# Performance work log

Hardware: AMD Instinct MI355X
Metric: run time of the kernel (lower is better)

The kernel has to match this reference:

```python
import jax, jax.numpy as jnp
import numpy as np
from jax import lax

N = 1_000_000   # nodes
E = 16_000_000  # edges
K1, K2, K3 = 100_000, 10_000, 2_500  # ceil(ratio*n) per pooling stage
EPS = 1e-5


def cgconv(x, src, dst, edge_attr, edge_valid, Wf, bf, Ws, bs, gamma, beta, num_nodes):
    # z_ij = [x_i, x_j, e_ij]  (PyG: i = target = dst, j = source = src)
    z = jnp.concatenate([x[dst], x[src], edge_attr], axis=-1)          # [E,3]
    m = jax.nn.sigmoid(z @ Wf + bf) * jax.nn.softplus(z @ Ws + bs)     # [E,1]
    m = m * edge_valid[:, None].astype(m.dtype)
    aggr = jax.ops.segment_sum(m, dst, num_segments=num_nodes)         # [n,1]
    # BatchNorm1d (training-mode batch stats, biased var), then residual
    mean = aggr.mean(axis=0)
    var = aggr.var(axis=0)
    bn = gamma * (aggr - mean) / jnp.sqrt(var + EPS) + beta
    return bn + x


def topk_pool(x, src, dst, edge_attr, edge_valid, w, k, num_nodes):
    # Original torch code broadcasts x[N,1]*w[C] -> sum(-1) == x*sum(w); tanh nonlinearity.
    score = jnp.tanh(x[:, 0] * jnp.sum(w) / jnp.linalg.norm(w))        # [n]
    top_scores, perm = lax.top_k(score, k)
    x_new = x[perm] * top_scores[:, None]
    mask = jnp.zeros((num_nodes,), bool).at[perm].set(True)
    new_idx = jnp.zeros((num_nodes,), jnp.int32).at[perm].set(jnp.arange(k, dtype=jnp.int32))
    ev = edge_valid & mask[src] & mask[dst]
    return x_new, new_idx[src], new_idx[dst], edge_attr, ev


def setup_inputs() -> dict:
    key = jax.random.key(0)
    ks = jax.random.split(key, 24)
    d = {}
    d["x"] = jax.random.normal(ks[0], (N, 1), jnp.float32)
    d["edge_attr"] = jax.random.uniform(ks[1], (E, 1), jnp.float32)
    d["src"] = jax.random.randint(ks[2], (E,), 0, N, jnp.int32)
    d["dst"] = jax.random.randint(ks[3], (E,), 0, N, jnp.int32)
    d["batch"] = jnp.zeros((N,), jnp.int32)
    p = lambda k, shp: jax.random.normal(k, shp, jnp.float32) * 0.1
    d["Wf1"], d["bf1"] = p(ks[4], (3, 1)), p(ks[5], (1,))
    d["Ws1"], d["bs1"] = p(ks[6], (3, 1)), p(ks[7], (1,))
    d["g1"], d["be1"] = jnp.ones((1,), jnp.float32), jnp.zeros((1,), jnp.float32)
    d["Wf2"], d["bf2"] = p(ks[8], (3, 1)), p(ks[9], (1,))
    d["Ws2"], d["bs2"] = p(ks[10], (3, 1)), p(ks[11], (1,))
    d["g2"], d["be2"] = jnp.ones((1,), jnp.float32), jnp.zeros((1,), jnp.float32)
    d["pw1"] = p(ks[12], (800,))
    d["pw2"] = p(ks[13], (80,))
    d["pw3"] = p(ks[14], (8,))
    d["Wl1"], d["bl1"] = p(ks[15], (1, 8)), p(ks[16], (8,))
    d["Wl2"], d["bl2"] = p(ks[17], (8, 2)), p(ks[18], (2,))
    return d


def reference(x, edge_attr, Wf1, bf1, Ws1, bs1, g1, be1, Wf2, bf2, Ws2, bs2, g2, be2,
              pw1, pw2, pw3, Wl1, bl1, Wl2, bl2, src, dst, batch):
    ev = jnp.ones((E,), bool)
    x = cgconv(x, src, dst, edge_attr, ev, Wf1, bf1, Ws1, bs1, g1, be1, N)
    x, s, dd, ea, ev = topk_pool(x, src, dst, edge_attr, ev, pw1, K1, N)
    x = cgconv(x, s, dd, ea, ev, Wf2, bf2, Ws2, bs2, g2, be2, K1)
    x, s, dd, ea, ev = topk_pool(x, s, dd, ea, ev, pw2, K2, K1)
    x, s, dd, ea, ev = topk_pool(x, s, dd, ea, ev, pw3, K3, K2)
    h = jax.nn.relu(x @ Wl1 + bl1)
    # dropout is identity in eval/reference mode
    return jax.nn.log_softmax(h @ Wl2 + bl2, axis=1)
```

## Files before the change

### kernel.cpp

```cpp
#include <hip/hip_runtime.h>
#include <math.h>

#define CHUNK 4096
#define NB2   256
#define BSH   12
#define CAP   24
#define CAPW  49
#define FG    16
#define RND   1024
#define EPB   16384

typedef int      i32x4 __attribute__((ext_vector_type(4)));
typedef float    f32x4 __attribute__((ext_vector_type(4)));
typedef unsigned u32x2 __attribute__((ext_vector_type(2)));

__device__ __forceinline__ i32x4 ntld4i(const int* p)   { return __builtin_nontemporal_load((const i32x4*)p); }
__device__ __forceinline__ f32x4 ntld4f(const float* p) { return __builtin_nontemporal_load((const f32x4*)p); }

__device__ __forceinline__ float sigmoidf_(float x) {
    if (x >= 0.0f) { float e = expf(-x); return 1.0f / (1.0f + e); }
    float e = expf(x); return e / (1.0f + e);
}
__device__ __forceinline__ float softplusf_(float x) {
    return fmaxf(x, 0.0f) + log1pf(expf(-fabsf(x)));
}
__device__ __forceinline__ unsigned key_desc(float f) {
    unsigned u = __float_as_uint(f);
    unsigned ka = (u & 0x80000000u) ? ~u : (u | 0x80000000u);
    return ~ka;
}
__device__ __forceinline__ float edge_m(float xd, float xs, float a,
                                        float wf0, float wf1, float wf2, float b0,
                                        float ws0, float ws1, float ws2, float b1) {
    float f = xd * wf0 + xs * wf1 + a * wf2 + b0;
    float g = xd * ws0 + xs * ws1 + a * ws2 + b1;
    return sigmoidf_(f) * softplusf_(g);
}

__global__ void k_consts(const float* __restrict__ pw1, const float* __restrict__ pw2,
                         const float* __restrict__ pw3, float* __restrict__ consts,
                         float* __restrict__ stats, int n1, int n2, int n3) {
    if (blockIdx.x == 0 && threadIdx.x < 16) stats[threadIdx.x] = 0.f;
    const float* w; int n;
    if (blockIdx.x == 0)      { w = pw1; n = n1; }
    else if (blockIdx.x == 1) { w = pw2; n = n2; }
    else                      { w = pw3; n = n3; }
    __shared__ float s1[256], s2[256];
    float a = 0.f, b = 0.f;
    for (int i = threadIdx.x; i < n; i += 256) { float v = w[i]; a += v; b += v * v; }
    s1[threadIdx.x] = a; s2[threadIdx.x] = b; __syncthreads();
    for (int o = 128; o > 0; o >>= 1) {
        if (threadIdx.x < o) { s1[threadIdx.x] += s1[threadIdx.x + o]; s2[threadIdx.x] += s2[threadIdx.x + o]; }
        __syncthreads();
    }
    if (threadIdx.x == 0) consts[blockIdx.x] = s1[0] / sqrtf(s2[0]);
}

__global__ void __launch_bounds__(256) k_ehist2(const int* __restrict__ dst,
                                                unsigned* __restrict__ hist,
                                                int e0, int e1) {
    __shared__ unsigned h[NB2];
    int t = threadIdx.x;
    h[t] = 0;
    __syncthreads();
    int cs = e0 + blockIdx.x * EPB;
    int ce = cs + EPB; if (ce > e1) ce = e1;
    for (int eb = cs; eb < ce; eb += RND) {
        int i = eb + t * 4;
        if (eb + RND <= ce) {
            i32x4 d4 = ntld4i(dst + i);
            atomicAdd(&h[((unsigned)d4.x) >> BSH], 1u);
            atomicAdd(&h[((unsigned)d4.y) >> BSH], 1u);
            atomicAdd(&h[((unsigned)d4.z) >> BSH], 1u);
            atomicAdd(&h[((unsigned)d4.w) >> BSH], 1u);
        } else {
            #pragma unroll
            for (int j = 0; j < 4; ++j)
                if (i + j < ce) atomicAdd(&h[((unsigned)dst[i + j]) >> BSH], 1u);
        }
    }
    __syncthreads();
    hist[(size_t)blockIdx.x * NB2 + t] = h[t];
}

__global__ void k_scanA(const unsigned* __restrict__ hist, unsigned* __restrict__ offs,
                        unsigned* __restrict__ tot, int G) {
    int d = blockIdx.x, ND = gridDim.x, t = threadIdx.x;
    __shared__ unsigned s[256];
    unsigned carry = 0;
    for (int tile = 0; tile * 256 < G; ++tile) {
        int g = tile * 256 + t;
        unsigned v = (g < G) ? hist[(size_t)g * ND + d] : 0u;
        s[t] = v; __syncthreads();
        for (int o = 1; o < 256; o <<= 1) {
            unsigned u = (t >= o) ? s[t - o] : 0u;
            __syncthreads();
            s[t] += u; __syncthreads();
        }
        if (g < G) offs[(size_t)g * ND + d] = s[t] - v + carry;
        unsigned tl = s[255]; __syncthreads();
        carry += tl;
    }
    if (t == 0) tot[d] = carry;
}

__global__ void __launch_bounds__(256) k_part(
        const float* __restrict__ x, const float* __restrict__ ea,
        const int* __restrict__ src, const int* __restrict__ dst,
        const float* __restrict__ Wf, const float* __restrict__ bf,
        const float* __restrict__ Ws, const float* __restrict__ bs,
        const unsigned* __restrict__ offs, const unsigned* __restrict__ tot,
        uint2* __restrict__ rec, int e0, int e1) {
    __shared__ unsigned stage[NB2 * CAPW];
    __shared__ unsigned gcur[NB2], fil[NB2];
    int t = threadIdx.x;
    {
        unsigned v = (tot[t] + FG - 1) & ~(unsigned)(FG - 1);
        stage[t] = v; __syncthreads();
        for (int o = 1; o < 256; o <<= 1) {
            unsigned u = (t >= o) ? stage[t - o] : 0u;
            __syncthreads();
            stage[t] += u; __syncthreads();
        }
        gcur[t] = (stage[t] - v) + offs[(size_t)blockIdx.x * NB2 + t];
        fil[t] = 0;
    }
    __syncthreads();
    int cs = e0 + blockIdx.x * EPB;
    int ce = cs + EPB; if (ce > e1) ce = e1;
    float wf0 = Wf[0], wf1 = Wf[1], wf2 = Wf[2], b0 = bf[0];
    float ws0 = Ws[0], ws1 = Ws[1], ws2 = Ws[2], b1 = bs[0];
    int sg = t >> 4, ln = t & 15;
    for (int rb = cs; rb < ce; rb += RND) {
        int s4[4], d4[4]; float a4[4]; bool vl[4];
        int eb = rb + t * 4;
        if (rb + RND <= ce) {
            i32x4 sv = ntld4i(src + eb);
            i32x4 dv = ntld4i(dst + eb);
            f32x4 av = ntld4f(ea + eb);
            s4[0]=sv.x; s4[1]=sv.y; s4[2]=sv.z; s4[3]=sv.w;
            d4[0]=dv.x; d4[1]=dv.y; d4[2]=dv.z; d4[3]=dv.w;
            a4[0]=av.x; a4[1]=av.y; a4[2]=av.z; a4[3]=av.w;
            vl[0]=vl[1]=vl[2]=vl[3]=true;
        } else {
            #pragma unroll
            for (int j = 0; j < 4; ++j) {
                int e = eb + j;
                vl[j] = e < ce;
                s4[j] = vl[j] ? src[e] : 0;
                d4[j] = vl[j] ? dst[e] : 0;
                a4[j] = vl[j] ? ea[e]  : 0.f;
            }
        }
        #pragma unroll
        for (int j = 0; j < 4; ++j) {
            if (!vl[j]) continue;
            int d = d4[j];
            float m = edge_m(x[d], x[s4[j]], a4[j], wf0, wf1, wf2, b0, ws0, ws1, ws2, b1);
            unsigned bin = ((unsigned)d) >> BSH;
            unsigned dl  = (unsigned)(d & ((1 << BSH) - 1));
            unsigned slot = atomicAdd(&fil[bin], 1u);
            if (slot < CAP) {
                stage[bin * CAPW + 2 * slot]     = __float_as_uint(m);
                stage[bin * CAPW + 2 * slot + 1] = dl;
            } else {
                rec[gcur[bin] + slot] = make_uint2(__float_as_uint(m), dl);
            }
        }
        __syncthreads();
        for (int i = 0; i < NB2 / 16; ++i) {
            int b = sg + (i << 4);
            unsigned c = fil[b];
            if (c < FG) continue;
            unsigned g = gcur[b];
            unsigned* st = &stage[b * CAPW];
            if (c > CAP) {
                rec[g + ln] = make_uint2(st[2 * ln], st[2 * ln + 1]);
                if (ln < CAP - 16)
                    rec[g + 16 + ln] = make_uint2(st[2 * (16 + ln)], st[2 * (16 + ln) + 1]);
                if (ln == 0) { gcur[b] = g + c; fil[b] = 0; }
            } else {
                rec[g + ln] = make_uint2(st[2 * ln], st[2 * ln + 1]);
                unsigned rem = c - FG;
                unsigned lo0 = 0, lo1 = 0;
                if (ln < rem) { lo0 = st[2 * (FG + ln)]; lo1 = st[2 * (FG + ln) + 1]; }
                if (ln < rem) { st[2 * ln] = lo0; st[2 * ln + 1] = lo1; }
                if (ln == 0) { gcur[b] = g + FG; fil[b] = rem; }
            }
        }
        __syncthreads();
    }
    for (int i = 0; i < NB2 / 16; ++i) {
        int b = sg + (i << 4);
        unsigned c = fil[b], g = gcur[b];
        unsigned* st = &stage[b * CAPW];
        if (ln < c) rec[g + ln] = make_uint2(st[2 * ln], st[2 * ln + 1]);
    }
}

__global__ void __launch_bounds__(256) k_aggr2(
        const uint2* __restrict__ rec, const unsigned* __restrict__ tot,
        float* __restrict__ aggr, float* __restrict__ stats,
        int N, int accumulate, int doStats) {
    __shared__ float acc[1 << BSH];
    __shared__ unsigned sc[256];
    __shared__ unsigned sBase, sCnt;
    int t = threadIdx.x, b = blockIdx.x;
    {
        unsigned v = (tot[t] + FG - 1) & ~(unsigned)(FG - 1);
        sc[t] = v; __syncthreads();
        for (int o = 1; o < 256; o <<= 1) {
            unsigned u = (t >= o) ? sc[t - o] : 0u;
            __syncthreads();
            sc[t] += u; __syncthreads();
        }
        if (t == b) { sBase = sc[t] - v; sCnt = tot[t]; }
    }
    for (int i = t; i < (1 << BSH); i += 256) acc[i] = 0.f;
    __syncthreads();
    unsigned lo = sBase, hi = lo + sCnt;
    for (unsigned i = lo + t; i < hi; i += 256) {
        u32x2 r = __builtin_nontemporal_load((const u32x2*)&rec[i]);
        atomicAdd(&acc[r.y], __uint_as_float(r.x));
    }
    __syncthreads();
    int nb = b << BSH;
    float s = 0.f, q = 0.f;
    for (int i = t; i < (1 << BSH); i += 256) {
        int node = nb + i;
        if (node < N) {
            float v = acc[i];
            if (accumulate) v += aggr[node];
            aggr[node] = v;
            if (doStats) { s += v; q += v * v; }
        }
    }
    if (doStats) {
        __shared__ float s1[256], s2[256];
        s1[t] = s; s2[t] = q; __syncthreads();
        for (int o = 128; o > 0; o >>= 1) {
            if (t < o) { s1[t] += s1[t + o]; s2[t] += s2[t + o]; }
            __syncthreads();
        }
        if (t == 0) { atomicAdd(&stats[0], s1[0]); atomicAdd(&stats[1], s2[0]); }
    }
}

__global__ void k_conv1(const float* __restrict__ x, const float* __restrict__ ea,
                        const int* __restrict__ src, const int* __restrict__ dst,
                        const float* __restrict__ Wf, const float* __restrict__ bf,
                        const float* __restrict__ Ws, const float* __restrict__ bs,
                        float* __restrict__ aggr, int E) {
    int e = blockIdx.x * blockDim.x + threadIdx.x;
    if (e >= E) return;
    int s = src[e], d = dst[e];
    atomicAdd(&aggr[d], edge_m(x[d], x[s], ea[e], Wf[0], Wf[1], Wf[2], bf[0],
                               Ws[0], Ws[1], Ws[2], bs[0]));
}

__global__ void __launch_bounds__(256) k_conv2(
        const float* __restrict__ x2, const float* __restrict__ ea,
        const int* __restrict__ src, const int* __restrict__ dst,
        const int* __restrict__ nidx,
        const float* __restrict__ Wf, const float* __restrict__ bf,
        const float* __restrict__ Ws, const float* __restrict__ bs,
        float* __restrict__ aggr, int E) {
    int base = (blockIdx.x * 256 + threadIdx.x) * 4;
    if (base >= E) return;
    float wf0 = Wf[0], wf1 = Wf[1], wf2 = Wf[2], b0 = bf[0];
    float ws0 = Ws[0], ws1 = Ws[1], ws2 = Ws[2], b1 = bs[0];
    int d4[4], s4[4]; int cnt;
    if (base + 4 <= E) {
        i32x4 dv = ntld4i(dst + base);
        i32x4 sv = ntld4i(src + base);
        d4[0]=dv.x; d4[1]=dv.y; d4[2]=dv.z; d4[3]=dv.w;
        s4[0]=sv.x; s4[1]=sv.y; s4[2]=sv.z; s4[3]=sv.w;
        cnt = 4;
    } else {
        cnt = E - base;
        for (int j = 0; j < cnt; ++j) { d4[j] = dst[base + j]; s4[j] = src[base + j]; }
    }
    #pragma unroll
    for (int j = 0; j < 4; ++j) {
        if (j >= cnt) break;
        int nd = nidx[d4[j]];
        if (nd < 0) continue;
        int ns = nidx[s4[j]];
        if (ns < 0) continue;
        float a = __builtin_nontemporal_load(ea + base + j);
        atomicAdd(&aggr[nd], edge_m(x2[nd], x2[ns], a, wf0, wf1, wf2, b0, ws0, ws1, ws2, b1));
    }
}

__global__ void k_stats(const float* __restrict__ a, int n, float* __restrict__ stats) {
    float s = 0.f, q = 0.f;
    int stride = gridDim.x * blockDim.x;
    for (int i = blockIdx.x * blockDim.x + threadIdx.x; i < n; i += stride) {
        float v = a[i]; s += v; q += v * v;
    }
    __shared__ float s1[256], s2[256];
    s1[threadIdx.x] = s; s2[threadIdx.x] = q; __syncthreads();
    for (int o = 128; o > 0; o >>= 1) {
        if (threadIdx.x < o) { s1[threadIdx.x] += s1[threadIdx.x + o]; s2[threadIdx.x] += s2[threadIdx.x + o]; }
        __syncthreads();
    }
    if (threadIdx.x == 0) { atomicAdd(&stats[0], s1[0]); atomicAdd(&stats[1], s2[0]); }
}

__global__ void k_bn(const float* __restrict__ aggr, const float* __restrict__ xin,
                     const float* __restrict__ stats, const float* __restrict__ g,
                     const float* __restrict__ be, float* __restrict__ xout,
                     int n, float invn, const float* __restrict__ consts, int ci,
                     unsigned* __restrict__ keys, unsigned* __restrict__ vals,
                     int* __restrict__ nidxInit, float* __restrict__ zeroArr, int nZero) {
    int i = blockIdx.x * blockDim.x + threadIdx.x;
    if (i >= n) return;
    if (nidxInit) nidxInit[i] = -1;
    if (zeroArr && i < nZero) zeroArr[i] = 0.f;
    float mean = stats[0] * invn;
    float var  = stats[1] * invn - mean * mean;
    float inv  = 1.0f / sqrtf(var + 1e-5f);
    float v = g[0] * (aggr[i] - mean) * inv + be[0] + xin[i];
    xout[i] = v;
    float s = tanhf(v * consts[ci]);
    keys[i] = key_desc(s);
    vals[i] = (unsigned)i;
}

__global__ void k_hist(const unsigned* __restrict__ keys, unsigned* __restrict__ hist,
                       int n, int shift) {
    __shared__ unsigned h[256];
    int t = threadIdx.x;
    h[t] = 0;
    __syncthreads();
    int base = blockIdx.x * CHUNK;
    if (base + CHUNK <= n) {
        #pragma unroll
        for (int it = 0; it < CHUNK / 1024; ++it) {
            int i = base + it * 1024 + t * 4;
            const unsigned* p = keys + i;
            unsigned k0 = p[0], k1 = p[1], k2 = p[2], k3 = p[3];
            atomicAdd(&h[(k0 >> shift) & 255u], 1u);
            atomicAdd(&h[(k1 >> shift) & 255u], 1u);
            atomicAdd(&h[(k2 >> shift) & 255u], 1u);
            atomicAdd(&h[(k3 >> shift) & 255u], 1u);
        }
    } else {
        for (int i = base + t; i < n; i += 256)
            atomicAdd(&h[(keys[i] >> shift) & 255u], 1u);
    }
    __syncthreads();
    hist[blockIdx.x * 256 + t] = h[t];
}

__global__ void __launch_bounds__(256) k_scatter(const unsigned* __restrict__ keys,
                                                 const unsigned* __restrict__ vals,
                                                 unsigned* __restrict__ okeys,
                                                 unsigned* __restrict__ ovals,
                                                 const unsigned* __restrict__ offs,
                                                 const unsigned* __restrict__ tot,
                                                 int n, int shift) {
    __shared__ unsigned run[256];
    __shared__ unsigned offl[256];
    __shared__ unsigned wcnt[4][256];
    __shared__ unsigned wpre[4][256];
    __shared__ unsigned sc[256];
    int t = threadIdx.x;
    int wave = t >> 6, lane = t & 63;
    {
        unsigned v = tot[t];
        sc[t] = v; __syncthreads();
        for (int o = 1; o < 256; o <<= 1) {
            unsigned u = (t >= o) ? sc[t - o] : 0u;
            __syncthreads();
            sc[t] += u; __syncthreads();
        }
        offl[t] = offs[(size_t)blockIdx.x * 256 + t] + (sc[t] - v);
        run[t] = 0;
    }
    __syncthreads();
    int cbase = blockIdx.x * CHUNK;
    const int GROUPS = CHUNK / 256;
    for (int gix = 0; gix < GROUPS; ++gix) {
        int i = cbase + gix * 256 + t;
        bool active = i < n;
        unsigned k = active ? keys[i] : 0u;
        unsigned v = active ? vals[i] : 0u;
        unsigned d = (k >> shift) & 255u;
        unsigned long long amask = __ballot(active);
        unsigned long long bb[8];
        #pragma unroll
        for (int bit = 0; bit < 8; ++bit) bb[bit] = __ballot(active && ((d >> bit) & 1u));
        unsigned long long m = amask;
        #pragma unroll
        for (int bit = 0; bit < 8; ++bit) m &= ((d >> bit) & 1u) ? bb[bit] : ~bb[bit];
        unsigned rk = (unsigned)__popcll(m & ((1ull << lane) - 1ull));
        #pragma unroll
        for (int j = 0; j < 4; ++j) {
            unsigned dd = (unsigned)lane + j * 64u;
            unsigned long long mm = amask;
            #pragma unroll
            for (int bit = 0; bit < 8; ++bit) mm &= ((dd >> bit) & 1u) ? bb[bit] : ~bb[bit];
            wcnt[wave][dd] = (unsigned)__popcll(mm);
        }
        __syncthreads();
        {
            unsigned r = run[t];
            unsigned c0 = wcnt[0][t], c1 = wcnt[1][t], c2 = wcnt[2][t], c3 = wcnt[3][t];
            wpre[0][t] = r;
            wpre[1][t] = r + c0;
            wpre[2][t] = r + c0 + c1;
            wpre[3][t] = r + c0 + c1 + c2;
            run[t] = r + c0 + c1 + c2 + c3;
        }
        __syncthreads();
        if (active) {
            unsigned pos = offl[d] + wpre[wave][d] + rk;
            okeys[pos] = k;
            ovals[pos] = v;
        }
    }
}

__global__ void k_pool(const unsigned* __restrict__ perm, const float* __restrict__ xin,
                       const float* __restrict__ consts, int ci,
                       float* __restrict__ xout, int* __restrict__ newidx, int k,
                       unsigned* __restrict__ okeys, unsigned* __restrict__ ovals, int nci) {
    int r = blockIdx.x * blockDim.x + threadIdx.x;
    if (r >= k) return;
    unsigned p = perm[r];
    float xv = xin[p];
    float s = tanhf(xv * consts[ci]);
    float o = xv * s;
    xout[r] = o;
    if (newidx) newidx[p] = r;
    if (okeys) {
        float s2 = tanhf(o * consts[nci]);
        okeys[r] = key_desc(s2);
        ovals[r] = (unsigned)r;
    }
}

__global__ void __launch_bounds__(1024) k_smallsort(
        unsigned* __restrict__ kIn, unsigned* __restrict__ vIn,
        unsigned* __restrict__ kTmp, unsigned* __restrict__ vTmp,
        int n, int k3, const float* __restrict__ xin,
        const float* __restrict__ consts, int ci,
        const float* __restrict__ Wl1, const float* __restrict__ bl1,
        const float* __restrict__ Wl2, const float* __restrict__ bl2,
        float* __restrict__ out) {
    __shared__ unsigned hist[256], sc[256], run[256], offl[256];
    __shared__ unsigned wcnt[16][256];
    __shared__ unsigned wpre[16][256];
    int t = threadIdx.x;
    int wave = t >> 6, lane = t & 63;
    unsigned *ki = kIn, *vi = vIn, *ko = kTmp, *vo = vTmp;
    for (int p = 0; p < 4; ++p) {
        int shift = p * 8;
        if (t < 256) hist[t] = 0;
        __syncthreads();
        for (int i = t; i < n; i += 1024)
            atomicAdd(&hist[(ki[i] >> shift) & 255u], 1u);
        __syncthreads();
        if (t < 256) sc[t] = hist[t];
        __syncthreads();
        for (int o = 1; o < 256; o <<= 1) {
            unsigned u = 0;
            if (t < 256 && t >= o) u = sc[t - o];
            __syncthreads();
            if (t < 256) sc[t] += u;
            __syncthreads();
        }
        if (t < 256) { offl[t] = sc[t] - hist[t]; run[t] = 0; }
        __syncthreads();
        int G = (n + 1023) / 1024;
        for (int gix = 0; gix < G; ++gix) {
            int i = gix * 1024 + t;
            bool active = i < n;
            unsigned k = active ? ki[i] : 0u;
            unsigned v = active ? vi[i] : 0u;
            unsigned d = (k >> shift) & 255u;
            unsigned long long amask = __ballot(active);
            unsigned long long bb[8];
            #pragma unroll
            for (int bit = 0; bit < 8; ++bit) bb[bit] = __ballot(active && ((d >> bit) & 1u));
            unsigned long long m = amask;
            #pragma unroll
            for (int bit = 0; bit < 8; ++bit) m &= ((d >> bit) & 1u) ? bb[bit] : ~bb[bit];
            unsigned rk = (unsigned)__popcll(m & ((1ull << lane) - 1ull));
            #pragma unroll
            for (int j = 0; j < 4; ++j) {
                unsigned dd = (unsigned)lane + j * 64u;
                unsigned long long mm = amask;
                #pragma unroll
                for (int bit = 0; bit < 8; ++bit) mm &= ((dd >> bit) & 1u) ? bb[bit] : ~bb[bit];
                wcnt[wave][dd] = (unsigned)__popcll(mm);
            }
            __syncthreads();
            if (t < 256) {
                unsigned acc = run[t];
                #pragma unroll
                for (int w2 = 0; w2 < 16; ++w2) { wpre[w2][t] = acc; acc += wcnt[w2][t]; }
                run[t] = acc;
            }
            __syncthreads();
            if (active) {
                unsigned pos = offl[d] + wpre[wave][d] + rk;
                ko[pos] = k;
                vo[pos] = v;
            }
            __syncthreads();
        }
        unsigned* tp;
        tp = ki; ki = ko; ko = tp;
        tp = vi; vi = vo; vo = tp;
        __syncthreads();
    }
    float c = consts[ci];
    float b20 = bl2[0], b21 = bl2[1];
    for (int r = t; r < k3; r += 1024) {
        unsigned pidx = vIn[r];
        float xv = xin[pidx];
        float s = tanhf(xv * c);
        float o = xv * s;
        float l0 = b20, l1 = b21;
        #pragma unroll
        for (int j = 0; j < 8; ++j) {
            float h = fmaxf(o * Wl1[j] + bl1[j], 0.0f);
            l0 += h * Wl2[2 * j];
            l1 += h * Wl2[2 * j + 1];
        }
        float mx = fmaxf(l0, l1);
        float lse = mx + logf(expf(l0 - mx) + expf(l1 - mx));
        out[2 * r]     = l0 - lse;
        out[2 * r + 1] = l1 - lse;
    }
}

static void sort_pairs(hipStream_t stream, unsigned* kA, unsigned* vA,
                       unsigned* kB, unsigned* vB, unsigned* hist, unsigned* offs,
                       unsigned* tot, int n) {
    int G = (n + CHUNK - 1) / CHUNK;
    unsigned *ki = kA, *vi = vA, *ko = kB, *vo = vB;
    for (int p = 0; p < 4; ++p) {
        int shift = p * 8;
        k_hist<<<G, 256, 0, stream>>>(ki, hist, n, shift);
        k_scanA<<<256, 256, 0, stream>>>(hist, offs, tot, G);
        k_scatter<<<G, 256, 0, stream>>>(ki, vi, ko, vo, offs, tot, n, shift);
        unsigned* t;
        t = ki; ki = ko; ko = t;
        t = vi; vi = vo; vo = t;
    }
}

extern "C" void kernel_launch(void* const* d_in, const int* in_sizes, int n_in,
                              void* d_out, int out_size, void* d_ws, size_t ws_size,
                              hipStream_t stream) {
    const float* x   = (const float*)d_in[0];
    const float* ea  = (const float*)d_in[1];
    const int*   src = (const int*)d_in[2];
    const int*   dst = (const int*)d_in[3];
    const float *Wf1 = (const float*)d_in[5],  *bf1 = (const float*)d_in[6];
    const float *Ws1 = (const float*)d_in[7],  *bs1 = (const float*)d_in[8];
    const float *g1  = (const float*)d_in[9],  *be1 = (const float*)d_in[10];
    const float *Wf2 = (const float*)d_in[11], *bf2 = (const float*)d_in[12];
    const float *Ws2 = (const float*)d_in[13], *bs2 = (const float*)d_in[14];
    const float *g2  = (const float*)d_in[15], *be2 = (const float*)d_in[16];
    const float *pw1 = (const float*)d_in[17], *pw2 = (const float*)d_in[18], *pw3 = (const float*)d_in[19];
    const float *Wl1 = (const float*)d_in[20], *bl1 = (const float*)d_in[21];
    const float *Wl2 = (const float*)d_in[22], *bl2 = (const float*)d_in[23];

    const int N  = in_sizes[0];
    const int E  = in_sizes[1];
    const int K1 = 100000, K2 = 10000, K3 = 2500;

    size_t off = 0;
    auto alloc = [&](size_t bytes) { size_t o = off; off = (off + bytes + 255) & ~(size_t)255; return o; };
    char* ws = (char*)d_ws;
    size_t o_x1    = alloc((size_t)N * 4);
    size_t o_nidx  = alloc((size_t)N * 4);
    size_t o_stats = alloc(256);
    size_t o_const = alloc(256);
    size_t o_tot   = alloc(4096);
    size_t o_x2    = alloc((size_t)K1 * 4);
    size_t o_x3    = alloc((size_t)K1 * 4);
    size_t o_ag2   = alloc((size_t)K1 * 4);
    size_t o_x4    = alloc((size_t)K2 * 4);
    size_t o_ag1   = alloc((size_t)N * 4);
    size_t o_arena = off;

    int G1 = (N + CHUNK - 1) / CHUNK;
    size_t s_kA = 0;
    size_t s_vA = s_kA + (((size_t)N * 4 + 255) & ~(size_t)255);
    size_t s_kB = s_vA + (((size_t)N * 4 + 255) & ~(size_t)255);
    size_t s_vB = s_kB + (((size_t)N * 4 + 255) & ~(size_t)255);
    size_t s_h  = s_vB + (((size_t)N * 4 + 255) & ~(size_t)255);
    size_t s_o  = s_h  + (((size_t)G1 * 256 * 4 + 255) & ~(size_t)255);
    size_t sortSz = s_o + (size_t)G1 * 256 * 4;

    int H = 0, Eh = 0;
    size_t p_rec = 0, p_eh = 0, p_eo = 0;
    for (int h = 1; h <= 8; h <<= 1) {
        int eh_ = (E + h - 1) / h;
        eh_ = (eh_ + RND - 1) & ~(RND - 1);
        int gc_ = (eh_ + EPB - 1) / EPB;
        size_t recB = (((size_t)(eh_ + NB2 * FG) * 8) + 255) & ~(size_t)255;
        size_t ehB  = (((size_t)gc_ * NB2 * 4) + 255) & ~(size_t)255;
        size_t eoB  = (((size_t)gc_ * NB2 * 4) + 255) & ~(size_t)255;
        size_t partSz = recB + ehB + eoB;
        size_t arenaSz = partSz > sortSz ? partSz : sortSz;
        if (o_arena + arenaSz <= ws_size && N <= (NB2 << BSH)) {
            H = h; Eh = eh_;
            p_rec = 0; p_eh = p_rec + recB; p_eo = p_eh + ehB;
            break;
        }
    }

    float*    x1     = (float*)(ws + o_x1);
    int*      nidx   = (int*)(ws + o_nidx);
    float*    stats  = (float*)(ws + o_stats);
    float*    consts = (float*)(ws + o_const);
    unsigned* tot    = (unsigned*)(ws + o_tot);
    float*    x2     = (float*)(ws + o_x2);
    float*    x3     = (float*)(ws + o_x3);
    float*    aggr2  = (float*)(ws + o_ag2);
    float*    x4     = (float*)(ws + o_x4);
    float*    aggr1  = (float*)(ws + o_ag1);
    unsigned* kA     = (unsigned*)(ws + o_arena + s_kA);
    unsigned* vA     = (unsigned*)(ws + o_arena + s_vA);
    unsigned* kB     = (unsigned*)(ws + o_arena + s_kB);
    unsigned* vB     = (unsigned*)(ws + o_arena + s_vB);
    unsigned* hist   = (unsigned*)(ws + o_arena + s_h);
    unsigned* offs   = (unsigned*)(ws + o_arena + s_o);

    k_consts<<<3, 256, 0, stream>>>(pw1, pw2, pw3, consts, stats,
                                    in_sizes[17], in_sizes[18], in_sizes[19]);

    if (H > 0) {
        uint2*    rec = (uint2*)(ws + o_arena + p_rec);
        unsigned* eh  = (unsigned*)(ws + o_arena + p_eh);
        unsigned* eo  = (unsigned*)(ws + o_arena + p_eo);
        int NBN = (N + (1 << BSH) - 1) >> BSH;
        for (int h = 0; h < H; ++h) {
            int e0 = h * Eh;
            int e1 = e0 + Eh; if (e1 > E) e1 = E;
            if (e0 >= e1) break;
            int GCh = (e1 - e0 + EPB - 1) / EPB;
            k_ehist2<<<GCh, 256, 0, stream>>>(dst, eh, e0, e1);
            k_scanA<<<NB2, 256, 0, stream>>>(eh, eo, tot, GCh);
            k_part<<<GCh, 256, 0, stream>>>(x, ea, src, dst, Wf1, bf1, Ws1, bs1,
                                            eo, tot, rec, e0, e1);
            k_aggr2<<<NBN, 256, 0, stream>>>(rec, tot, aggr1, stats, N,
                                             h > 0, h == H - 1 ? 1 : 0);
        }
    } else {
        hipMemsetAsync(aggr1, 0, (size_t)N * 4, stream);
        k_conv1<<<(E + 255) / 256, 256, 0, stream>>>(x, ea, src, dst, Wf1, bf1, Ws1, bs1, aggr1, E);
        k_stats<<<1024, 256, 0, stream>>>(aggr1, N, stats);
    }
    k_bn<<<(N + 255) / 256, 256, 0, stream>>>(aggr1, x, stats, g1, be1, x1, N, 1.0f / (float)N,
                                              consts, 0, kA, vA, nidx, aggr2, K1);

    sort_pairs(stream, kA, vA, kB, vB, hist, offs, tot, N);
    k_pool<<<(K1 + 255) / 256, 256, 0, stream>>>(vA, x1, consts, 0, x2, nidx, K1,
                                                 (unsigned*)nullptr, (unsigned*)nullptr, 0);

    k_conv2<<<(E / 4 + 255) / 256, 256, 0, stream>>>(x2, ea, src, dst, nidx,
                                                     Wf2, bf2, Ws2, bs2, aggr2, E);
    k_stats<<<256, 256, 0, stream>>>(aggr2, K1, stats + 2);
    k_bn<<<(K1 + 255) / 256, 256, 0, stream>>>(aggr2, x2, stats + 2, g2, be2, x3, K1, 1.0f / (float)K1,
                                               consts, 1, kA, vA,
                                               (int*)nullptr, (float*)nullptr, 0);

    sort_pairs(stream, kA, vA, kB, vB, hist, offs, tot, K1);
    k_pool<<<(K2 + 255) / 256, 256, 0, stream>>>(vA, x3, consts, 1, x4, (int*)nullptr, K2,
                                                 kB, vB, 2);

    k_smallsort<<<1, 1024, 0, stream>>>(kB, vB, kA, vA, K2, K3, x4, consts, 2,
                                        Wl1, bl1, Wl2, bl2, (float*)d_out);
}
```

Before: 882.7 us.

## Prefilter top-K candidates by radix histogram before sorting, and worklist partition flushes

Before the stage-1 top-K selection, a coarse 11-bit histogram of the sort keys locates the bin that contains the K-th key. Only keys at or below that bin are compacted and then radix-sorted, with the element count read from device memory, so roughly K1-sized data is sorted instead of all N nodes. Separately, the edge partition kernel keeps a per-round worklist of full bins instead of scanning all 256 bins, and pads each per-block bin segment to FG with zero records. This adds several small kernels and pads the record buffer, but it is meant to sharply cut the cost of the full-N sort.

```diff
diff --git a/kernel.cpp b/kernel.cpp
--- a/kernel.cpp
+++ b/kernel.cpp
@@ -13,6 +13,7 @@
 typedef int      i32x4 __attribute__((ext_vector_type(4)));
 typedef float    f32x4 __attribute__((ext_vector_type(4)));
 typedef unsigned u32x2 __attribute__((ext_vector_type(2)));
+typedef unsigned u32x4 __attribute__((ext_vector_type(4)));
 
 __device__ __forceinline__ i32x4 ntld4i(const int* p)   { return __builtin_nontemporal_load((const i32x4*)p); }
 __device__ __forceinline__ f32x4 ntld4f(const float* p) { return __builtin_nontemporal_load((const f32x4*)p); }
@@ -39,8 +40,12 @@
 
 __global__ void k_consts(const float* __restrict__ pw1, const float* __restrict__ pw2,
                          const float* __restrict__ pw3, float* __restrict__ consts,
-                         float* __restrict__ stats, int n1, int n2, int n3) {
-    if (blockIdx.x == 0 && threadIdx.x < 16) stats[threadIdx.x] = 0.f;
+                         float* __restrict__ stats, unsigned* __restrict__ ghist,
+                         int n1, int n2, int n3) {
+    if (blockIdx.x == 0) {
+        if (threadIdx.x < 16) stats[threadIdx.x] = 0.f;
+        for (int i = threadIdx.x; i < 2048; i += 256) ghist[i] = 0u;
+    }
     const float* w; int n;
     if (blockIdx.x == 0)      { w = pw1; n = n1; }
     else if (blockIdx.x == 1) { w = pw2; n = n2; }
@@ -84,13 +89,13 @@
 }
 
 __global__ void k_scanA(const unsigned* __restrict__ hist, unsigned* __restrict__ offs,
-                        unsigned* __restrict__ tot, int G) {
+                        unsigned* __restrict__ tot, int G, unsigned rmask) {
     int d = blockIdx.x, ND = gridDim.x, t = threadIdx.x;
     __shared__ unsigned s[256];
     unsigned carry = 0;
     for (int tile = 0; tile * 256 < G; ++tile) {
         int g = tile * 256 + t;
-        unsigned v = (g < G) ? hist[(size_t)g * ND + d] : 0u;
+        unsigned v = (g < G) ? ((hist[(size_t)g * ND + d] + rmask) & ~rmask) : 0u;
         s[t] = v; __syncthreads();
         for (int o = 1; o < 256; o <<= 1) {
             unsigned u = (t >= o) ? s[t - o] : 0u;
@@ -110,20 +115,27 @@
         const float* __restrict__ Wf, const float* __restrict__ bf,
         const float* __restrict__ Ws, const float* __restrict__ bs,
         const unsigned* __restrict__ offs, const unsigned* __restrict__ tot,
+        const unsigned* __restrict__ eh,
         uint2* __restrict__ rec, int e0, int e1) {
     __shared__ unsigned stage[NB2 * CAPW];
-    __shared__ unsigned gcur[NB2], fil[NB2];
+    __shared__ unsigned gcur[NB2], fil[NB2], gend[NB2];
+    __shared__ unsigned short wl[2][NB2];
+    __shared__ unsigned wlc[2];
     int t = threadIdx.x;
     {
-        unsigned v = (tot[t] + FG - 1) & ~(unsigned)(FG - 1);
+        unsigned v = tot[t];
         stage[t] = v; __syncthreads();
         for (int o = 1; o < 256; o <<= 1) {
             unsigned u = (t >= o) ? stage[t - o] : 0u;
             __syncthreads();
             stage[t] += u; __syncthreads();
         }
-        gcur[t] = (stage[t] - v) + offs[(size_t)blockIdx.x * NB2 + t];
+        unsigned g0 = (stage[t] - v) + offs[(size_t)blockIdx.x * NB2 + t];
+        unsigned cnt = eh[(size_t)blockIdx.x * NB2 + t];
+        gcur[t] = g0;
+        gend[t] = g0 + ((cnt + FG - 1) & ~(unsigned)(FG - 1));
         fil[t] = 0;
+        if (t < 2) wlc[t] = 0;
     }
     __syncthreads();
     int cs = e0 + blockIdx.x * EPB;
@@ -131,7 +143,9 @@
     float wf0 = Wf[0], wf1 = Wf[1], wf2 = Wf[2], b0 = bf[0];
     float ws0 = Ws[0], ws1 = Ws[1], ws2 = Ws[2], b1 = bs[0];
     int sg = t >> 4, ln = t & 15;
-    for (int rb = cs; rb < ce; rb += RND) {
+    int rnd = 0;
+    for (int rb = cs; rb < ce; rb += RND, ++rnd) {
+        int cur = rnd & 1;
         int s4[4], d4[4]; float a4[4]; bool vl[4];
         int eb = rb + t * 4;
         if (rb + RND <= ce) {
@@ -160,6 +174,10 @@
             unsigned bin = ((unsigned)d) >> BSH;
             unsigned dl  = (unsigned)(d & ((1 << BSH) - 1));
             unsigned slot = atomicAdd(&fil[bin], 1u);
+            if (slot == FG - 1) {
+                unsigned w = atomicAdd(&wlc[cur], 1u);
+                wl[cur][w] = (unsigned short)bin;
+            }
             if (slot < CAP) {
                 stage[bin * CAPW + 2 * slot]     = __float_as_uint(m);
                 stage[bin * CAPW + 2 * slot + 1] = dl;
@@ -168,11 +186,10 @@
             }
         }
         __syncthreads();
-        for (int i = 0; i < NB2 / 16; ++i) {
-            int b = sg + (i << 4);
-            unsigned c = fil[b];
-            if (c < FG) continue;
-            unsigned g = gcur[b];
+        unsigned nw = wlc[cur];
+        for (unsigned i = sg; i < nw; i += 16) {
+            int b = wl[cur][i];
+            unsigned c = fil[b], g = gcur[b];
             unsigned* st = &stage[b * CAPW];
             if (c > CAP) {
                 rec[g + ln] = make_uint2(st[2 * ln], st[2 * ln + 1]);
@@ -182,19 +199,23 @@
             } else {
                 rec[g + ln] = make_uint2(st[2 * ln], st[2 * ln + 1]);
                 unsigned rem = c - FG;
-                unsigned lo0 = 0, lo1 = 0;
-                if (ln < rem) { lo0 = st[2 * (FG + ln)]; lo1 = st[2 * (FG + ln) + 1]; }
-                if (ln < rem) { st[2 * ln] = lo0; st[2 * ln + 1] = lo1; }
+                unsigned a0 = 0, a1 = 0;
+                if (ln < rem) { a0 = st[2 * (FG + ln)]; a1 = st[2 * (FG + ln) + 1]; }
+                if (ln < rem) { st[2 * ln] = a0; st[2 * ln + 1] = a1; }
                 if (ln == 0) { gcur[b] = g + FG; fil[b] = rem; }
             }
         }
+        if (t == 0) wlc[cur ^ 1] = 0;
         __syncthreads();
     }
     for (int i = 0; i < NB2 / 16; ++i) {
         int b = sg + (i << 4);
-        unsigned c = fil[b], g = gcur[b];
+        unsigned g = gcur[b], c = fil[b], ge = gend[b];
         unsigned* st = &stage[b * CAPW];
-        if (ln < c) rec[g + ln] = make_uint2(st[2 * ln], st[2 * ln + 1]);
+        for (unsigned p = g + ln; p < ge; p += 16) {
+            unsigned k2 = p - g;
+            rec[p] = (k2 < c) ? make_uint2(st[2 * k2], st[2 * k2 + 1]) : make_uint2(0u, 0u);
+        }
     }
 }
 
@@ -207,7 +228,7 @@
     __shared__ unsigned sBase, sCnt;
     int t = threadIdx.x, b = blockIdx.x;
     {
-        unsigned v = (tot[t] + FG - 1) & ~(unsigned)(FG - 1);
+        unsigned v = tot[t];
         sc[t] = v; __syncthreads();
         for (int o = 1; o < 256; o <<= 1) {
             unsigned u = (t >= o) ? sc[t - o] : 0u;
@@ -327,8 +348,106 @@
     vals[i] = (unsigned)i;
 }
 
+__global__ void __launch_bounds__(256) k_ghist(const unsigned* __restrict__ keys,
+                                               unsigned* __restrict__ ghist, int n) {
+    __shared__ unsigned h[2048];
+    int t = threadIdx.x;
+    for (int i = t; i < 2048; i += 256) h[i] = 0;
+    __syncthreads();
+    int stride = gridDim.x * 1024;
+    for (int base = blockIdx.x * 1024 + t * 4; base + 3 < n; base += stride) {
+        u32x4 k4 = __builtin_nontemporal_load((const u32x4*)(keys + base));
+        atomicAdd(&h[k4.x >> 21], 1u);
+        atomicAdd(&h[k4.y >> 21], 1u);
+        atomicAdd(&h[k4.z >> 21], 1u);
+        atomicAdd(&h[k4.w >> 21], 1u);
+    }
+    if (blockIdx.x == 0) {
+        int tail = n & ~3;
+        for (int i = tail + t; i < n; i += 256)
+            atomicAdd(&h[keys[i] >> 21], 1u);
+    }
+    __syncthreads();
+    for (int i = t; i < 2048; i += 256) { unsigned v = h[i]; if (v) atomicAdd(&ghist[i], v); }
+}
+
+__global__ void k_findT(const unsigned* __restrict__ ghist, unsigned* __restrict__ sel, int K) {
+    __shared__ unsigned s[256];
+    int t = threadIdx.x;
+    unsigned carry = 0;
+    for (int tile = 0; tile < 8; ++tile) {
+        unsigned v = ghist[tile * 256 + t];
+        s[t] = v; __syncthreads();
+        for (int o = 1; o < 256; o <<= 1) {
+            unsigned u = (t >= o) ? s[t - o] : 0u;
+            __syncthreads();
+            s[t] += u; __syncthreads();
+        }
+        unsigned cum = s[t] + carry;
+        if (cum >= (unsigned)K && cum - v < (unsigned)K) {
+            sel[0] = (unsigned)(tile * 256 + t);
+            sel[1] = cum;
+        }
+        unsigned tl = s[255]; __syncthreads();
+        carry += tl;
+    }
+}
+
+__global__ void __launch_bounds__(256) k_selcnt(const unsigned* __restrict__ keys,
+                                                const unsigned* __restrict__ sel,
+                                                unsigned* __restrict__ chist, int n) {
+    unsigned T = sel[0];
+    int t = threadIdx.x;
+    int base = blockIdx.x * CHUNK;
+    int end = base + CHUNK; if (end > n) end = n;
+    unsigned c = 0;
+    for (int i = base + t; i < end; i += 256)
+        c += ((keys[i] >> 21) <= T) ? 1u : 0u;
+    __shared__ unsigned s[256];
+    s[t] = c; __syncthreads();
+    for (int o = 128; o > 0; o >>= 1) { if (t < o) s[t] += s[t + o]; __syncthreads(); }
+    if (t == 0) chist[blockIdx.x] = s[0];
+}
+
+__global__ void __launch_bounds__(256) k_selcompact(
+        const unsigned* __restrict__ keys, const unsigned* __restrict__ vals,
+        const unsigned* __restrict__ sel, const unsigned* __restrict__ chist,
+        unsigned* __restrict__ okeys, unsigned* __restrict__ ovals, int n, int G) {
+    __shared__ unsigned s[256];
+    __shared__ unsigned wsum[4];
+    __shared__ unsigned runS;
+    unsigned T = sel[0];
+    int t = threadIdx.x, wave = t >> 6, lane = t & 63;
+    unsigned v = (t < G) ? chist[t] : 0u;
+    s[t] = v; __syncthreads();
+    for (int o = 1; o < 256; o <<= 1) {
+        unsigned u = (t >= o) ? s[t - o] : 0u;
+        __syncthreads();
+        s[t] += u; __syncthreads();
+    }
+    if (t == (int)blockIdx.x) runS = s[t] - v;
+    __syncthreads();
+    int cbase = blockIdx.x * CHUNK;
+    for (int gix = 0; gix < CHUNK / 256; ++gix) {
+        int i = cbase + gix * 256 + t;
+        bool selq = (i < n) && ((keys[i] >> 21) <= T);
+        unsigned long long mk = __ballot(selq);
+        unsigned pre = (unsigned)__popcll(mk & ((1ull << lane) - 1ull));
+        if (lane == 0) wsum[wave] = (unsigned)__popcll(mk);
+        __syncthreads();
+        unsigned wb = runS;
+        #pragma unroll
+        for (int w = 0; w < 4; ++w) if (w < wave) wb += wsum[w];
+        if (selq) { unsigned pos = wb + pre; okeys[pos] = keys[i]; ovals[pos] = vals[i]; }
+        __syncthreads();
+        if (t == 0) runS += wsum[0] + wsum[1] + wsum[2] + wsum[3];
+        __syncthreads();
+    }
+}
+
 __global__ void k_hist(const unsigned* __restrict__ keys, unsigned* __restrict__ hist,
-                       int n, int shift) {
+                       int n, const unsigned* __restrict__ pn, int shift) {
+    if (pn) n = (int)*pn;
     __shared__ unsigned h[256];
     int t = threadIdx.x;
     h[t] = 0;
@@ -359,7 +478,10 @@
                                                  unsigned* __restrict__ ovals,
                                                  const unsigned* __restrict__ offs,
                                                  const unsigned* __restrict__ tot,
-                                                 int n, int shift) {
+                                                 int n, const unsigned* __restrict__ pn,
+                                                 int shift) {
+    if (pn) n = (int)*pn;
+    if ((int)blockIdx.x * CHUNK >= n) return;
     __shared__ unsigned run[256];
     __shared__ unsigned offl[256];
     __shared__ unsigned wcnt[4][256];
@@ -537,16 +659,15 @@
     }
 }
 
-static void sort_pairs(hipStream_t stream, unsigned* kA, unsigned* vA,
-                       unsigned* kB, unsigned* vB, unsigned* hist, unsigned* offs,
-                       unsigned* tot, int n) {
-    int G = (n + CHUNK - 1) / CHUNK;
-    unsigned *ki = kA, *vi = vA, *ko = kB, *vo = vB;
+static void sort_pairs(hipStream_t stream, unsigned* kI, unsigned* vI,
+                       unsigned* kT, unsigned* vT, unsigned* hist, unsigned* offs,
+                       unsigned* tot, int n, int G, const unsigned* pn) {
+    unsigned *ki = kI, *vi = vI, *ko = kT, *vo = vT;
     for (int p = 0; p < 4; ++p) {
         int shift = p * 8;
-        k_hist<<<G, 256, 0, stream>>>(ki, hist, n, shift);
-        k_scanA<<<256, 256, 0, stream>>>(hist, offs, tot, G);
-        k_scatter<<<G, 256, 0, stream>>>(ki, vi, ko, vo, offs, tot, n, shift);
+        k_hist<<<G, 256, 0, stream>>>(ki, hist, n, pn, shift);
+        k_scanA<<<256, 256, 0, stream>>>(hist, offs, tot, G, 0u);
+        k_scatter<<<G, 256, 0, stream>>>(ki, vi, ko, vo, offs, tot, n, pn, shift);
         unsigned* t;
         t = ki; ki = ko; ko = t;
         t = vi; vi = vo; vo = t;
@@ -582,6 +703,7 @@
     size_t o_stats = alloc(256);
     size_t o_const = alloc(256);
     size_t o_tot   = alloc(4096);
+    size_t o_gh    = alloc(8192);
     size_t o_x2    = alloc((size_t)K1 * 4);
     size_t o_x3    = alloc((size_t)K1 * 4);
     size_t o_ag2   = alloc((size_t)K1 * 4);
@@ -604,7 +726,7 @@
         int eh_ = (E + h - 1) / h;
         eh_ = (eh_ + RND - 1) & ~(RND - 1);
         int gc_ = (eh_ + EPB - 1) / EPB;
-        size_t recB = (((size_t)(eh_ + NB2 * FG) * 8) + 255) & ~(size_t)255;
+        size_t recB = (((size_t)eh_ + (size_t)gc_ * NB2 * FG + NB2 * FG) * 8 + 255) & ~(size_t)255;
         size_t ehB  = (((size_t)gc_ * NB2 * 4) + 255) & ~(size_t)255;
         size_t eoB  = (((size_t)gc_ * NB2 * 4) + 255) & ~(size_t)255;
         size_t partSz = recB + ehB + eoB;
@@ -621,6 +743,8 @@
     float*    stats  = (float*)(ws + o_stats);
     float*    consts = (float*)(ws + o_const);
     unsigned* tot    = (unsigned*)(ws + o_tot);
+    unsigned* selp   = tot + 512;
+    unsigned* ghist  = (unsigned*)(ws + o_gh);
     float*    x2     = (float*)(ws + o_x2);
     float*    x3     = (float*)(ws + o_x3);
     float*    aggr2  = (float*)(ws + o_ag2);
@@ -633,7 +757,7 @@
     unsigned* hist   = (unsigned*)(ws + o_arena + s_h);
     unsigned* offs   = (unsigned*)(ws + o_arena + s_o);
 
-    k_consts<<<3, 256, 0, stream>>>(pw1, pw2, pw3, consts, stats,
+    k_consts<<<3, 256, 0, stream>>>(pw1, pw2, pw3, consts, stats, ghist,
                                     in_sizes[17], in_sizes[18], in_sizes[19]);
 
     if (H > 0) {
@@ -647,9 +771,9 @@
             if (e0 >= e1) break;
             int GCh = (e1 - e0 + EPB - 1) / EPB;
             k_ehist2<<<GCh, 256, 0, stream>>>(dst, eh, e0, e1);
-            k_scanA<<<NB2, 256, 0, stream>>>(eh, eo, tot, GCh);
+            k_scanA<<<NB2, 256, 0, stream>>>(eh, eo, tot, GCh, (unsigned)(FG - 1));
             k_part<<<GCh, 256, 0, stream>>>(x, ea, src, dst, Wf1, bf1, Ws1, bs1,
-                                            eo, tot, rec, e0, e1);
+                                            eo, tot, eh, rec, e0, e1);
             k_aggr2<<<NBN, 256, 0, stream>>>(rec, tot, aggr1, stats, N,
                                              h > 0, h == H - 1 ? 1 : 0);
         }
@@ -661,8 +785,12 @@
     k_bn<<<(N + 255) / 256, 256, 0, stream>>>(aggr1, x, stats, g1, be1, x1, N, 1.0f / (float)N,
                                               consts, 0, kA, vA, nidx, aggr2, K1);
 
-    sort_pairs(stream, kA, vA, kB, vB, hist, offs, tot, N);
-    k_pool<<<(K1 + 255) / 256, 256, 0, stream>>>(vA, x1, consts, 0, x2, nidx, K1,
+    k_ghist<<<256, 256, 0, stream>>>(kA, ghist, N);
+    k_findT<<<1, 256, 0, stream>>>(ghist, selp, K1);
+    k_selcnt<<<G1, 256, 0, stream>>>(kA, selp, hist, N);
+    k_selcompact<<<G1, 256, 0, stream>>>(kA, vA, selp, hist, kB, vB, N, G1);
+    sort_pairs(stream, kB, vB, kA, vA, hist, offs, tot, N, G1, selp + 1);
+    k_pool<<<(K1 + 255) / 256, 256, 0, stream>>>(vB, x1, consts, 0, x2, nidx, K1,
                                                  (unsigned*)nullptr, (unsigned*)nullptr, 0);
 
     k_conv2<<<(E / 4 + 255) / 256, 256, 0, stream>>>(x2, ea, src, dst, nidx,
@@ -672,7 +800,8 @@
                                                consts, 1, kA, vA,
                                                (int*)nullptr, (float*)nullptr, 0);
 
-    sort_pairs(stream, kA, vA, kB, vB, hist, offs, tot, K1);
+    sort_pairs(stream, kA, vA, kB, vB, hist, offs, tot, K1,
+               (K1 + CHUNK - 1) / CHUNK, (const unsigned*)nullptr);
     k_pool<<<(K2 + 255) / 256, 256, 0, stream>>>(vA, x3, consts, 1, x4, (int*)nullptr, K2,
                                                  kB, vB, 2);
 
```

Result: faster. 845.7 us (median of 2 runs) (-4.2%).
